# Kernel optimization log

Hardware: AMD Instinct MI355X
Metric: run time of the kernel (lower is better)

The kernel has to match this reference:

```python
import jax, jax.numpy as jnp
from jax import lax
import numpy as np

B = 32768
N_IN = 8
N_HID = 64
N_CTRL = 2
M_SCEN = (1.0, 1.2)          # scenario parameters for f/g
M_NOM = 1.0
CLF_LAM = 1.0
CBF_LAM = 1.0
P_CLF = 100.0
P_CBF = 50.0
QP_ITERS = 80                # fixed-iteration batched ADMM (OSQP-style) replacing CvxpyLayer
RHO = 1.0
SIGMA = 1e-6
INF = jnp.inf


def setup_inputs() -> dict:
    key = jax.random.key(0)
    ks = jax.random.split(key, 16)
    s = 0.3
    return {
        "x":   jax.random.normal(ks[0], (B, N_IN), jnp.float32),
        "VW1": jax.random.normal(ks[1], (N_HID, N_IN), jnp.float32) * s,
        "Vb1": jax.random.normal(ks[2], (N_HID,), jnp.float32) * s,
        "VW2": jax.random.normal(ks[3], (N_HID, N_HID), jnp.float32) * s,
        "Vb2": jax.random.normal(ks[4], (N_HID,), jnp.float32) * s,
        "HW1": jax.random.normal(ks[5], (N_HID, N_IN), jnp.float32) * s,
        "Hb1": jax.random.normal(ks[6], (N_HID,), jnp.float32) * s,
        "HW2": jax.random.normal(ks[7], (N_HID, N_HID), jnp.float32) * s,
        "Hb2": jax.random.normal(ks[8], (N_HID,), jnp.float32) * s,
        "HW3": jax.random.normal(ks[9], (N_HID, N_HID), jnp.float32) * s,
        "Hb3": jax.random.normal(ks[10], (N_HID,), jnp.float32) * s,
        "HW4": jax.random.normal(ks[11], (1, N_HID), jnp.float32) * s,
        "Hb4": jax.random.normal(ks[12], (1,), jnp.float32) * s,
        "G0":  jax.random.normal(ks[13], (N_IN, N_CTRL), jnp.float32) * s,
        "K":   jax.random.normal(ks[14], (N_IN, N_CTRL), jnp.float32) * s,
    }


def _lyapunov(x, W1, b1, W2, b2):
    t1 = jnp.tanh(x @ W1.T + b1)                                   # [B,H]
    t2 = jnp.tanh(t1 @ W2.T + b2)                                  # [B,H]
    V = 0.5 * jnp.sum(t2 * t2, axis=1)                             # [B]
    # fused diag(1-t^2) @ W chain (no diag_embed materialization)
    D1 = (1.0 - t1 ** 2)[:, :, None] * W1[None]                    # [B,H,N]
    D2 = (1.0 - t2 ** 2)[:, :, None] * jnp.einsum('hk,bkn->bhn', W2, D1)
    grad_V = jnp.einsum('bh,bhn->bn', t2, D2)                      # [B,N]
    return V, grad_V


def _barrier(x, W1, b1, W2, b2, W3, b3, W4, b4):
    t1 = jnp.tanh(x @ W1.T + b1)
    t2 = jnp.tanh(t1 @ W2.T + b2)
    t3 = jnp.tanh(t2 @ W3.T + b3)
    H = t3 @ W4.T + b4                                             # [B,1]
    D1 = (1.0 - t1 ** 2)[:, :, None] * W1[None]
    D2 = (1.0 - t2 ** 2)[:, :, None] * jnp.einsum('hk,bkn->bhn', W2, D1)
    D3 = (1.0 - t3 ** 2)[:, :, None] * jnp.einsum('hk,bkn->bhn', W3, D2)
    grad_H = jnp.einsum('oh,bhn->bn', W4, D3)                      # [B,N] (o=1)
    return H, grad_H


def _solve_qp(q, A, lo, hi):
    """Batched OSQP-style ADMM for min 0.5 z^T P z + q^T z  s.t. lo <= A z <= hi.
    P = diag([2,2,0,0,0,0]); z = [u(2), r_clf(2), s_cbf(2)]. Fixed iterations."""
    nb, mc, nz = A.shape[0], A.shape[1], A.shape[2]
    Pdiag = jnp.array([2.0, 2.0, 0.0, 0.0, 0.0, 0.0], q.dtype)
    M = RHO * jnp.einsum('bmi,bmj->bij', A, A) + jnp.diag(Pdiag + SIGMA)
    Minv = jnp.linalg.inv(M)                                       # [B,6,6]
    x0 = jnp.zeros((nb, nz), q.dtype)
    z0 = jnp.zeros((nb, mc), q.dtype)
    y0 = jnp.zeros((nb, mc), q.dtype)

    def step(carry, _):
        xx, zz, yy = carry
        rhs = SIGMA * xx - q + jnp.einsum('bmi,bm->bi', A, RHO * zz - yy)
        xt = jnp.einsum('bij,bj->bi', Minv, rhs)
        zt = jnp.einsum('bmi,bi->bm', A, xt)
        zn = jnp.clip(zt + yy / RHO, lo, hi)
        yn = yy + RHO * (zt - zn)
        return (xt, zn, yn), None

    (xf, _, _), _ = lax.scan(step, (x0, z0, y0), None, length=QP_ITERS)
    return xf                                                      # [B,6]


def _forward(x, VW1, Vb1, VW2, Vb2, HW1, Hb1, HW2, Hb2, HW3, Hb3, HW4, Hb4, G0, K):
    V, grad_V = _lyapunov(x, VW1, Vb1, VW2, Vb2)
    H, grad_H = _barrier(x, HW1, Hb1, HW2, Hb2, HW3, Hb3, HW4, Hb4)

    LfVs, LgVs, LfHs, LgHs = [], [], [], []
    for m in M_SCEN:
        # f(x,m) = -x/m ; g(x,m) = G0/m
        LfVs.append(-jnp.sum(grad_V * x, axis=1) / m)              # [B]
        LgVs.append((grad_V @ G0) / m)                             # [B,C]
        LfHs.append(-jnp.sum(grad_H * x, axis=1) / m)
        LgHs.append((grad_H @ G0) / m)
    u_nom = -(x @ K) * (1.0 / M_NOM)                               # [B,C]

    nb = x.shape[0]
    z2 = jnp.zeros((nb, 2), x.dtype)
    ey = jnp.eye(2, dtype=x.dtype)
    e = lambda i: jnp.broadcast_to(ey[i], (nb, 2))
    ninf = jnp.full((nb,), -INF, x.dtype)
    pinf = jnp.full((nb,), INF, x.dtype)
    zer = jnp.zeros((nb,), x.dtype)

    rows, los, his = [], [], []
    for i in range(len(M_SCEN)):
        # CBF: LfH + LgH@u + cbf_lam*H + s_i >= 0
        rows.append(jnp.concatenate([LgHs[i], z2, e(i)], axis=1))
        los.append(-(LfHs[i] + CBF_LAM * H[:, 0])); his.append(pinf)
        # CLF: LfV + LgV@u + clf_lam*V - r_i <= 0
        rows.append(jnp.concatenate([LgVs[i], -e(i), z2], axis=1))
        los.append(ninf); his.append(-(LfVs[i] + CLF_LAM * V))
    for i in range(len(M_SCEN)):
        rows.append(jnp.concatenate([z2, e(i), z2], axis=1)); los.append(zer); his.append(pinf)
    for i in range(len(M_SCEN)):
        rows.append(jnp.concatenate([z2, z2, e(i)], axis=1)); los.append(zer); his.append(pinf)

    A = jnp.stack(rows, axis=1)                                    # [B,8,6]
    lo = jnp.stack(los, axis=1)                                    # [B,8]
    hi = jnp.stack(his, axis=1)
    # objective ||u-u_nom||^2 + p_clf*sum r + p_cbf*sum s  ->  q = [-2 u_nom, p_clf, p_clf, p_cbf, p_cbf]
    q = jnp.concatenate([-2.0 * u_nom,
                         jnp.full((nb, 2), P_CLF, x.dtype),
                         jnp.full((nb, 2), P_CBF, x.dtype)], axis=1)

    z = _solve_qp(q, A, lo, hi)                                    # [B,6]
    u = z[:, :N_CTRL]
    relaxation = jnp.mean(z[:, N_CTRL:N_CTRL + len(M_SCEN)], axis=1, keepdims=True)  # [B,1]

    ns = float(len(M_SCEN))
    Vdot = sum(LfVs[i] + jnp.sum(LgVs[i] * u, axis=1) for i in range(len(M_SCEN))) / ns
    Hdot = sum(LfHs[i] + jnp.sum(LgHs[i] * u, axis=1) for i in range(len(M_SCEN))) / ns
    return u, relaxation, V, Vdot[:, None, None], H, Hdot[:, None, None]


def reference(x, VW1, Vb1, VW2, Vb2, HW1, Hb1, HW2, Hb2, HW3, Hb3, HW4, Hb4, G0, K):
    return _forward(x, VW1, Vb1, VW2, Vb2, HW1, Hb1, HW2, Hb2, HW3, Hb3, HW4, Hb4, G0, K)
```

## Files before the change

kernel.cpp:

```cpp
#include <hip/hip_runtime.h>
#include <hip/hip_bf16.h>
#include <math.h>

#define BTOT 32768

typedef _Float16 f16x8 __attribute__((ext_vector_type(8)));
typedef _Float16 f16x4 __attribute__((ext_vector_type(4)));
typedef float    f32x4 __attribute__((ext_vector_type(4)));

#define LDS_FENCE() asm volatile("s_waitcnt lgkmcnt(0)" ::: "memory")

__device__ __forceinline__ float ldin(const void* p, int i, int f32f) {
  return f32f ? ((const float*)p)[i]
              : __bfloat162float(((const __hip_bfloat16*)p)[i]);
}

__device__ __forceinline__ f32x4 MFMA(f16x8 a, f16x8 b, f32x4 c) {
  return __builtin_amdgcn_mfma_f32_16x16x32_f16(a, b, c, 0, 0, 0);
}

__device__ __forceinline__ float tanh_fast(float x) {
  float e = __expf(2.f * x);
  return 1.f - 2.f / (e + 1.f);
}

__device__ __forceinline__ float redq(float v) {
  v += __shfl_xor(v, 16, 64);
  v += __shfl_xor(v, 32, 64);
  return v;
}

__device__ __forceinline__ int widx(int h, int k) {
  return ((h >> 4) << 10) + ((k >> 5) << 9) + (((k >> 3) & 3) << 7) + ((h & 15) << 3) + (k & 7);
}

__global__ __launch_bounds__(512, 2) void nn_kernel(
    const void* px, const void* pVW1, const void* pVb1, const void* pVW2, const void* pVb2,
    const void* pHW1, const void* pHb1, const void* pHW2, const void* pHb2,
    const void* pHW3, const void* pHb3, const void* pHW4, const void* pHb4,
    const void* pG0, const void* pK, float* WS, float* out)
{
  __shared__ __align__(16) _Float16 sVW2[4096], sVW2T[4096];
  __shared__ __align__(16) _Float16 sHW2[4096], sHW2T[4096];
  __shared__ __align__(16) _Float16 sHW3[4096], sHW3T[4096];
  __shared__ __align__(16) _Float16 sW1Vh[512], sW1Vl[512], sW1Hh[512], sW1Hl[512];
  __shared__ __align__(16) _Float16 sXh[1024], sXl[1024];
  __shared__ __align__(16) _Float16 sAVh[8][1024], sAVl[8][1024];
  __shared__ __align__(16) _Float16 sAHh[8][1024], sAHl[8][1024];
  __shared__ __align__(16) float sVb1[64], sVb2[64], sHb1[64], sHb2[64], sHb3[64], sW4[64];
  __shared__ __align__(16) float sWGV0[64], sWGV1[64], sWGH0[64], sWGH1[64];
  __shared__ float sHb4v;
  __shared__ int sCnt;

  const int tid = threadIdx.x, lane = tid & 63, wave = tid >> 6;
  const int m = lane & 15, q = lane >> 4;
  const int ro = q * 128 + m * 8;

  if (tid == 0) sCnt = 0;
  __syncthreads();
  {
    const unsigned short* xb = (const unsigned short*)px;
    int good = 0;
#pragma unroll
    for (int i = 0; i < 2; ++i) {
      int ex = (xb[tid * 2 + i] >> 7) & 0xFF;
      good += (ex >= 97 && ex <= 157) ? 1 : 0;
    }
    atomicAdd(&sCnt, good);
  }
  __syncthreads();
  const int f32f = (sCnt >= 870) ? 0 : 1;
  const bool wsplit = (f32f != 0);

  for (int i = tid; i < 4096; i += 512) {
    int h = i >> 6, k = i & 63;
    int fw = widx(h, k), tw = widx(k, h);
    sVW2[fw] = (_Float16)ldin(pVW2, i, f32f); sVW2T[tw] = sVW2[fw];
    sHW2[fw] = (_Float16)ldin(pHW2, i, f32f); sHW2T[tw] = sHW2[fw];
    sHW3[fw] = (_Float16)ldin(pHW3, i, f32f); sHW3T[tw] = sHW3[fw];
  }
  for (int i = tid; i < 512; i += 512) {
    float v = ldin(pVW1, i, f32f); _Float16 hh = (_Float16)v;
    sW1Vh[i] = hh; sW1Vl[i] = (_Float16)(v - (float)hh);
    v = ldin(pHW1, i, f32f); hh = (_Float16)v;
    sW1Hh[i] = hh; sW1Hl[i] = (_Float16)(v - (float)hh);
  }
  for (int i = tid; i < 1024; i += 512) {
    float v = ldin(px, blockIdx.x * 1024 + i, f32f); _Float16 hh = (_Float16)v;
    sXh[i] = hh; sXl[i] = (_Float16)(v - (float)hh);
  }
  if (tid < 64) {
    float a0 = 0.f, a1 = 0.f, b0 = 0.f, b1 = 0.f;
#pragma unroll
    for (int nn = 0; nn < 8; ++nn) {
      float g0 = ldin(pG0, 2 * nn, f32f), g1 = ldin(pG0, 2 * nn + 1, f32f);
      float wv = ldin(pVW1, tid * 8 + nn, f32f), wh = ldin(pHW1, tid * 8 + nn, f32f);
      a0 += wv * g0; a1 += wv * g1; b0 += wh * g0; b1 += wh * g1;
    }
    sWGV0[tid] = a0; sWGV1[tid] = a1; sWGH0[tid] = b0; sWGH1[tid] = b1;
    sVb1[tid] = ldin(pVb1, tid, f32f);
    sVb2[tid] = ldin(pVb2, tid, f32f);
    sHb1[tid] = ldin(pHb1, tid, f32f);
    sHb2[tid] = ldin(pHb2, tid, f32f);
    sHb3[tid] = ldin(pHb3, tid, f32f);
    sW4[tid]  = ldin(pHW4, tid, f32f);
  }
  if (tid == 0) sHb4v = ldin(pHb4, 0, f32f);
  __syncthreads();

  f16x8 zf;
#pragma unroll
  for (int i = 0; i < 8; ++i) zf[i] = (_Float16)0.f;

  _Float16 *aVh = sAVh[wave], *aVl = sAVl[wave];
  _Float16 *aHh = sAHh[wave], *aHl = sAHl[wave];
  const int tb = wave * 16;

  auto wgemm = [&](const _Float16* Wp, const _Float16* ah_, const _Float16* al_, f32x4* acc) {
    f16x8 b0h = *(const f16x8*)(ah_ + ro);
    f16x8 b1h = *(const f16x8*)(ah_ + 512 + ro);
    f16x8 b0l = *(const f16x8*)(al_ + ro);
    f16x8 b1l = *(const f16x8*)(al_ + 512 + ro);
#pragma unroll
    for (int ht = 0; ht < 4; ++ht) {
      const _Float16* ap = Wp + ht * 1024 + ro;
      f16x8 a0 = *(const f16x8*)ap, a1 = *(const f16x8*)(ap + 512);
      f32x4 c = {0.f, 0.f, 0.f, 0.f};
      c = MFMA(a0, b0h, c); c = MFMA(a1, b1h, c);
      c = MFMA(a0, b0l, c); c = MFMA(a1, b1l, c);
      acc[ht] = c;
    }
  };
  auto wstore = [&](const f32x4* vals, _Float16* ah_, _Float16* al_) {
#pragma unroll
    for (int ht = 0; ht < 4; ++ht) {
      int aw = ((ht >> 1) << 9) + (((ht & 1) * 2 + (q >> 1)) << 7) + m * 8 + ((q & 1) << 2);
      f16x4 vh, vl;
#pragma unroll
      for (int r = 0; r < 4; ++r) {
        float x = vals[ht][r];
        _Float16 hh = (_Float16)x;
        vh[r] = hh; vl[r] = (_Float16)(x - (float)hh);
      }
      *(f16x4*)(ah_ + aw) = vh;
      *(f16x4*)(al_ + aw) = vl;
    }
  };
  auto l1gemm = [&](const _Float16* W1h, const _Float16* W1l, f32x4* acc) {
    f16x8 xbh = zf, xbl = zf;
    if (lane < 16) {
      xbh = *(const f16x8*)(sXh + (tb + m) * 8);
      xbl = *(const f16x8*)(sXl + (tb + m) * 8);
    }
#pragma unroll
    for (int ht = 0; ht < 4; ++ht) {
      f16x8 afh = zf, afl = zf;
      if (lane < 16) {
        afh = *(const f16x8*)(W1h + (ht * 16 + m) * 8);
        afl = *(const f16x8*)(W1l + (ht * 16 + m) * 8);
      }
      f32x4 c = {0.f, 0.f, 0.f, 0.f};
      c = MFMA(afh, xbh, c);
      c = MFMA(afh, xbl, c);
      if (wsplit) c = MFMA(afl, xbh, c);
      acc[ht] = c;
    }
  };

  f32x4 accV[4], accH[4], z1V[4], z1H[4], d1V[4], d1H[4], d2H[4], tvV[4], tvH[4];

  l1gemm(sW1Vh, sW1Vl, accV);
  l1gemm(sW1Hh, sW1Hl, accH);
#pragma unroll
  for (int ht = 0; ht < 4; ++ht) {
    z1V[ht] = accV[ht]; z1H[ht] = accH[ht];
    f32x4 bV = *(const f32x4*)&sVb1[ht * 16 + q * 4];
    f32x4 bH = *(const f32x4*)&sHb1[ht * 16 + q * 4];
#pragma unroll
    for (int r = 0; r < 4; ++r) {
      float t = tanh_fast(z1V[ht][r] + bV[r]);
      tvV[ht][r] = t; d1V[ht][r] = 1.f - t * t;
      t = tanh_fast(z1H[ht][r] + bH[r]);
      tvH[ht][r] = t; d1H[ht][r] = 1.f - t * t;
    }
  }
  wstore(tvV, aVh, aVl);
  wstore(tvH, aHh, aHl);
  LDS_FENCE();

  wgemm(sVW2, aVh, aVl, accV);
  wgemm(sHW2, aHh, aHl, accH);
  float pV = 0.f;
#pragma unroll
  for (int ht = 0; ht < 4; ++ht) {
    f32x4 bV = *(const f32x4*)&sVb2[ht * 16 + q * 4];
    f32x4 bH = *(const f32x4*)&sHb2[ht * 16 + q * 4];
#pragma unroll
    for (int r = 0; r < 4; ++r) {
      float t = tanh_fast(accV[ht][r] + bV[r]);
      pV += t * t;
      tvV[ht][r] = t * (1.f - t * t);
      t = tanh_fast(accH[ht][r] + bH[r]);
      tvH[ht][r] = t; d2H[ht][r] = 1.f - t * t;
    }
  }
  wstore(tvV, aVh, aVl);
  wstore(tvH, aHh, aHl);
  LDS_FENCE();

  wgemm(sVW2T, aVh, aVl, accV);
  wgemm(sHW3, aHh, aHl, accH);
  float pgvx = 0.f, plv0 = 0.f, plv1 = 0.f, pH = 0.f;
#pragma unroll
  for (int ht = 0; ht < 4; ++ht) {
    f32x4 g0 = *(const f32x4*)&sWGV0[ht * 16 + q * 4];
    f32x4 g1 = *(const f32x4*)&sWGV1[ht * 16 + q * 4];
    f32x4 bH = *(const f32x4*)&sHb3[ht * 16 + q * 4];
    f32x4 w4 = *(const f32x4*)&sW4[ht * 16 + q * 4];
#pragma unroll
    for (int r = 0; r < 4; ++r) {
      float wt = accV[ht][r] * d1V[ht][r];
      pgvx += wt * z1V[ht][r];
      plv0 += wt * g0[r]; plv1 += wt * g1[r];
      float t = tanh_fast(accH[ht][r] + bH[r]);
      pH += t * w4[r];
      tvH[ht][r] = w4[r] * (1.f - t * t);
    }
  }
  wstore(tvH, aHh, aHl);
  LDS_FENCE();

  wgemm(sHW3T, aHh, aHl, accH);
#pragma unroll
  for (int ht = 0; ht < 4; ++ht)
#pragma unroll
    for (int r = 0; r < 4; ++r) tvH[ht][r] = accH[ht][r] * d2H[ht][r];
  wstore(tvH, aHh, aHl);
  LDS_FENCE();

  wgemm(sHW2T, aHh, aHl, accH);
  float pghx = 0.f, plh0 = 0.f, plh1 = 0.f;
#pragma unroll
  for (int ht = 0; ht < 4; ++ht) {
    f32x4 g0 = *(const f32x4*)&sWGH0[ht * 16 + q * 4];
    f32x4 g1 = *(const f32x4*)&sWGH1[ht * 16 + q * 4];
#pragma unroll
    for (int r = 0; r < 4; ++r) {
      float wt = accH[ht][r] * d1H[ht][r];
      pghx += wt * z1H[ht][r];
      plh0 += wt * g0[r]; plh1 += wt * g1[r];
    }
  }

  {
    float rgvx = redq(pgvx), rlv0 = redq(plv0), rlv1 = redq(plv1), rV = 0.5f * redq(pV);
    float rghx = redq(pghx), rlh0 = redq(plh0), rlh1 = redq(plh1), rH = redq(pH) + sHb4v;
    if (lane < 16) {
      int e = blockIdx.x * 128 + tb + lane;
      WS[0 * BTOT + e] = rlh0;  WS[1 * BTOT + e] = rlh1;
      WS[2 * BTOT + e] = rlv0;  WS[3 * BTOT + e] = rlv1;
      WS[4 * BTOT + e] = rghx;  WS[5 * BTOT + e] = rgvx;
      out[98304 + e]  = rV;
      out[163840 + e] = rH;
    }
  }
}

__global__ __launch_bounds__(64) void qp_kernel(const void* px, const void* pK,
                                                const float* WS, float* out) {
  __shared__ int sCnt;
  const int tid = threadIdx.x;
  if (tid == 0) sCnt = 0;
  __syncthreads();
  {
    const unsigned short* xb = (const unsigned short*)px;
    int good = 0;
#pragma unroll
    for (int i = 0; i < 2; ++i) {
      int ex = (xb[tid * 2 + i] >> 7) & 0xFF;
      good += (ex >= 97 && ex <= 157) ? 1 : 0;
    }
    atomicAdd(&sCnt, good);
  }
  __syncthreads();
  const int f32f = (sCnt >= 109) ? 0 : 1;

  const int e = blockIdx.x * 64 + tid;
  const float im = 1.0f / 1.2f;
  const float sg = 1e-6f;

  float gh0 = WS[0 * BTOT + e], gh1 = WS[1 * BTOT + e];
  float gv0 = WS[2 * BTOT + e], gv1 = WS[3 * BTOT + e];
  float ghx = WS[4 * BTOT + e], gvx = WS[5 * BTOT + e];
  float V = out[98304 + e], H = out[163840 + e];

  float un0 = 0.f, un1 = 0.f;
#pragma unroll
  for (int n = 0; n < 8; ++n) {
    float xv = ldin(px, e * 8 + n, f32f);
    un0 -= xv * ldin(pK, 2 * n, f32f);
    un1 -= xv * ldin(pK, 2 * n + 1, f32f);
  }

  float lo0 = ghx - H;
  float hi1 = gvx - V;
  float lo2 = ghx * im - H;
  float hi3 = gvx * im - V;
  float qv0 = -2.f * un0, qv1 = -2.f * un1;

  const float d  = 2.f + sg;
  const float rd = 1.f / d;
  const float al = 1.f + im * im;
  const float be = al * (1.f - rd);
  float S00 = be * (gh0 * gh0 + gv0 * gv0) + d;
  float S11 = be * (gh1 * gh1 + gv1 * gv1) + d;
  float S01 = be * (gh0 * gh1 + gv0 * gv1);
  float idet = 1.f / (S00 * S11 - S01 * S01);
  float i00 = S11 * idet, i11 = S00 * idet, i01 = -S01 * idet;

  float X0 = 0.f, X1 = 0.f, X2 = 0.f, X3 = 0.f, X4 = 0.f, X5 = 0.f;
  float Z[8] = {0.f, 0.f, 0.f, 0.f, 0.f, 0.f, 0.f, 0.f};
  float Y[8] = {0.f, 0.f, 0.f, 0.f, 0.f, 0.f, 0.f, 0.f};

#pragma unroll 1
  for (int it = 0; it < 80; ++it) {
    float t0 = Z[0] - Y[0], t1 = Z[1] - Y[1], t2 = Z[2] - Y[2], t3 = Z[3] - Y[3];
    float t4 = Z[4] - Y[4], t5 = Z[5] - Y[5], t6 = Z[6] - Y[6], t7 = Z[7] - Y[7];
    float tauh = t0 + im * t2, tauv = t1 + im * t3;
    float b0 = sg * X0 - qv0 + gh0 * tauh + gv0 * tauv;
    float b1 = sg * X1 - qv1 + gh1 * tauh + gv1 * tauv;
    float b2 = sg * X2 - 100.f - t1 + t4;
    float b3 = sg * X3 - 100.f - t3 + t5;
    float b4 = sg * X4 - 50.f + t0 + t6;
    float b5 = sg * X5 - 50.f + t2 + t7;
    float p  = b2 + im * b3;
    float s2 = b4 + im * b5;
    float cb0 = gh0 * s2 - gv0 * p;
    float cb1 = gh1 * s2 - gv1 * p;
    float u0b = b0 - cb0 * rd;
    float u1b = b1 - cb1 * rd;
    X0 = i00 * u0b + i01 * u1b;
    X1 = i01 * u0b + i11 * u1b;
    float gdH = gh0 * X0 + gh1 * X1;
    float gdV = gv0 * X0 + gv1 * X1;
    X2 = (b2 + gdV) * rd;
    X3 = (b3 + im * gdV) * rd;
    X4 = (b4 - gdH) * rd;
    X5 = (b5 - im * gdH) * rd;
    float zt0 = gdH + X4;
    float zt1 = gdV - X2;
    float zt2 = gdH * im + X5;
    float zt3 = gdV * im - X3;

    float v, zn;
    v = zt0 + Y[0]; zn = fmaxf(v, lo0); Y[0] += zt0 - zn; Z[0] = zn;
    v = zt1 + Y[1]; zn = fminf(v, hi1); Y[1] += zt1 - zn; Z[1] = zn;
    v = zt2 + Y[2]; zn = fmaxf(v, lo2); Y[2] += zt2 - zn; Z[2] = zn;
    v = zt3 + Y[3]; zn = fminf(v, hi3); Y[3] += zt3 - zn; Z[3] = zn;
    v = X2 + Y[4];  zn = fmaxf(v, 0.f); Y[4] += X2 - zn;  Z[4] = zn;
    v = X3 + Y[5];  zn = fmaxf(v, 0.f); Y[5] += X3 - zn;  Z[5] = zn;
    v = X4 + Y[6];  zn = fmaxf(v, 0.f); Y[6] += X4 - zn;  Z[6] = zn;
    v = X5 + Y[7];  zn = fmaxf(v, 0.f); Y[7] += X5 - zn;  Z[7] = zn;
  }

  float relax = 0.5f * (X2 + X3);
  const float cc = 0.5f * (1.f + im);
  float Vdot = cc * (gv0 * X0 + gv1 * X1 - gvx);
  float Hdot = cc * (gh0 * X0 + gh1 * X1 - ghx);

  out[2 * e]      = X0;
  out[2 * e + 1]  = X1;
  out[65536 + e]  = relax;
  out[131072 + e] = Vdot;
  out[196608 + e] = Hdot;
}

extern "C" void kernel_launch(void* const* d_in, const int* in_sizes, int n_in,
                              void* d_out, int out_size, void* d_ws, size_t ws_size,
                              hipStream_t stream) {
  float* out = (float*)d_out;
  float* WS  = (float*)d_ws;
  nn_kernel<<<256, 512, 0, stream>>>(
      d_in[0], d_in[1], d_in[2], d_in[3], d_in[4],
      d_in[5], d_in[6], d_in[7], d_in[8],
      d_in[9], d_in[10], d_in[11], d_in[12],
      d_in[13], d_in[14], WS, out);
  qp_kernel<<<512, 64, 0, stream>>>(d_in[0], d_in[14], WS, out);
}
```

Measured before the change: 122.3 us.

## Fuse QP solve into NN kernel, drop hi/lo split activations, serialize V/H nets

```diff
diff --git a/kernel.cpp b/kernel.cpp
--- a/kernel.cpp
+++ b/kernel.cpp
@@ -21,7 +21,7 @@
 
 __device__ __forceinline__ float tanh_fast(float x) {
   float e = __expf(2.f * x);
-  return 1.f - 2.f / (e + 1.f);
+  return 1.f - 2.f * __builtin_amdgcn_rcpf(e + 1.f);
 }
 
 __device__ __forceinline__ float redq(float v) {
@@ -34,22 +34,21 @@
   return ((h >> 4) << 10) + ((k >> 5) << 9) + (((k >> 3) & 3) << 7) + ((h & 15) << 3) + (k & 7);
 }
 
-__global__ __launch_bounds__(512, 2) void nn_kernel(
+__global__ __launch_bounds__(512, 4) void fused_kernel(
     const void* px, const void* pVW1, const void* pVb1, const void* pVW2, const void* pVb2,
     const void* pHW1, const void* pHb1, const void* pHW2, const void* pHb2,
     const void* pHW3, const void* pHb3, const void* pHW4, const void* pHb4,
-    const void* pG0, const void* pK, float* WS, float* out)
+    const void* pG0, const void* pK, float* out)
 {
   __shared__ __align__(16) _Float16 sVW2[4096], sVW2T[4096];
   __shared__ __align__(16) _Float16 sHW2[4096], sHW2T[4096];
   __shared__ __align__(16) _Float16 sHW3[4096], sHW3T[4096];
   __shared__ __align__(16) _Float16 sW1Vh[512], sW1Vl[512], sW1Hh[512], sW1Hl[512];
-  __shared__ __align__(16) _Float16 sXh[1024], sXl[1024];
-  __shared__ __align__(16) _Float16 sAVh[8][1024], sAVl[8][1024];
-  __shared__ __align__(16) _Float16 sAHh[8][1024], sAHl[8][1024];
+  __shared__ __align__(16) _Float16 sAct[8][1024];
   __shared__ __align__(16) float sVb1[64], sVb2[64], sHb1[64], sHb2[64], sHb3[64], sW4[64];
   __shared__ __align__(16) float sWGV0[64], sWGV1[64], sWGH0[64], sWGH1[64];
-  __shared__ float sHb4v;
+  __shared__ __align__(16) float sQP[128][11];
+  __shared__ float sKv[16], sHb4v;
   __shared__ int sCnt;
 
   const int tid = threadIdx.x, lane = tid & 63, wave = tid >> 6;
@@ -84,10 +83,6 @@
     sW1Vh[i] = hh; sW1Vl[i] = (_Float16)(v - (float)hh);
     v = ldin(pHW1, i, f32f); hh = (_Float16)v;
     sW1Hh[i] = hh; sW1Hl[i] = (_Float16)(v - (float)hh);
-  }
-  for (int i = tid; i < 1024; i += 512) {
-    float v = ldin(px, blockIdx.x * 1024 + i, f32f); _Float16 hh = (_Float16)v;
-    sXh[i] = hh; sXl[i] = (_Float16)(v - (float)hh);
   }
   if (tid < 64) {
     float a0 = 0.f, a1 = 0.f, b0 = 0.f, b1 = 0.f;
@@ -105,6 +100,7 @@
     sHb3[tid] = ldin(pHb3, tid, f32f);
     sW4[tid]  = ldin(pHW4, tid, f32f);
   }
+  if (tid < 16) sKv[tid] = ldin(pK, tid, f32f);
   if (tid == 0) sHb4v = ldin(pHb4, 0, f32f);
   __syncthreads();
 
@@ -112,46 +108,43 @@
 #pragma unroll
   for (int i = 0; i < 8; ++i) zf[i] = (_Float16)0.f;
 
-  _Float16 *aVh = sAVh[wave], *aVl = sAVl[wave];
-  _Float16 *aHh = sAHh[wave], *aHl = sAHl[wave];
+  _Float16* act = sAct[wave];
   const int tb = wave * 16;
-
-  auto wgemm = [&](const _Float16* Wp, const _Float16* ah_, const _Float16* al_, f32x4* acc) {
-    f16x8 b0h = *(const f16x8*)(ah_ + ro);
-    f16x8 b1h = *(const f16x8*)(ah_ + 512 + ro);
-    f16x8 b0l = *(const f16x8*)(al_ + ro);
-    f16x8 b1l = *(const f16x8*)(al_ + 512 + ro);
+  const int e0 = blockIdx.x * 128 + tb;
+
+  f16x8 xbh = zf, xbl = zf;
+  if (lane < 16) {
+#pragma unroll
+    for (int n = 0; n < 8; ++n) {
+      float v = ldin(px, (e0 + m) * 8 + n, f32f);
+      _Float16 hh = (_Float16)v;
+      xbh[n] = hh; xbl[n] = (_Float16)(v - (float)hh);
+    }
+  }
+
+  auto wgemm = [&](const _Float16* Wp, f32x4* acc) {
+    f16x8 b0 = *(const f16x8*)(act + ro);
+    f16x8 b1 = *(const f16x8*)(act + 512 + ro);
 #pragma unroll
     for (int ht = 0; ht < 4; ++ht) {
       const _Float16* ap = Wp + ht * 1024 + ro;
-      f16x8 a0 = *(const f16x8*)ap, a1 = *(const f16x8*)(ap + 512);
       f32x4 c = {0.f, 0.f, 0.f, 0.f};
-      c = MFMA(a0, b0h, c); c = MFMA(a1, b1h, c);
-      c = MFMA(a0, b0l, c); c = MFMA(a1, b1l, c);
+      c = MFMA(*(const f16x8*)ap, b0, c);
+      c = MFMA(*(const f16x8*)(ap + 512), b1, c);
       acc[ht] = c;
     }
   };
-  auto wstore = [&](const f32x4* vals, _Float16* ah_, _Float16* al_) {
+  auto wstore = [&](const f32x4* vals) {
 #pragma unroll
     for (int ht = 0; ht < 4; ++ht) {
       int aw = ((ht >> 1) << 9) + (((ht & 1) * 2 + (q >> 1)) << 7) + m * 8 + ((q & 1) << 2);
-      f16x4 vh, vl;
-#pragma unroll
-      for (int r = 0; r < 4; ++r) {
-        float x = vals[ht][r];
-        _Float16 hh = (_Float16)x;
-        vh[r] = hh; vl[r] = (_Float16)(x - (float)hh);
-      }
-      *(f16x4*)(ah_ + aw) = vh;
-      *(f16x4*)(al_ + aw) = vl;
+      f16x4 vh;
+#pragma unroll
+      for (int r = 0; r < 4; ++r) vh[r] = (_Float16)vals[ht][r];
+      *(f16x4*)(act + aw) = vh;
     }
   };
   auto l1gemm = [&](const _Float16* W1h, const _Float16* W1l, f32x4* acc) {
-    f16x8 xbh = zf, xbl = zf;
-    if (lane < 16) {
-      xbh = *(const f16x8*)(sXh + (tb + m) * 8);
-      xbl = *(const f16x8*)(sXl + (tb + m) * 8);
-    }
 #pragma unroll
     for (int ht = 0; ht < 4; ++ht) {
       f16x8 afh = zf, afl = zf;
@@ -167,78 +160,97 @@
     }
   };
 
-  f32x4 accV[4], accH[4], z1V[4], z1H[4], d1V[4], d1H[4], d2H[4], tvV[4], tvH[4];
-
-  l1gemm(sW1Vh, sW1Vl, accV);
-  l1gemm(sW1Hh, sW1Hl, accH);
-#pragma unroll
-  for (int ht = 0; ht < 4; ++ht) {
-    z1V[ht] = accV[ht]; z1H[ht] = accH[ht];
-    f32x4 bV = *(const f32x4*)&sVb1[ht * 16 + q * 4];
-    f32x4 bH = *(const f32x4*)&sHb1[ht * 16 + q * 4];
-#pragma unroll
-    for (int r = 0; r < 4; ++r) {
-      float t = tanh_fast(z1V[ht][r] + bV[r]);
-      tvV[ht][r] = t; d1V[ht][r] = 1.f - t * t;
-      t = tanh_fast(z1H[ht][r] + bH[r]);
-      tvH[ht][r] = t; d1H[ht][r] = 1.f - t * t;
-    }
-  }
-  wstore(tvV, aVh, aVl);
-  wstore(tvH, aHh, aHl);
-  LDS_FENCE();
-
-  wgemm(sVW2, aVh, aVl, accV);
-  wgemm(sHW2, aHh, aHl, accH);
+  f32x4 acc[4], z1[4], d1[4], d2[4], tv[4];
+
+  l1gemm(sW1Vh, sW1Vl, acc);
+#pragma unroll
+  for (int ht = 0; ht < 4; ++ht) {
+    z1[ht] = acc[ht];
+    f32x4 b4 = *(const f32x4*)&sVb1[ht * 16 + q * 4];
+#pragma unroll
+    for (int r = 0; r < 4; ++r) {
+      float t = tanh_fast(z1[ht][r] + b4[r]);
+      tv[ht][r] = t; d1[ht][r] = 1.f - t * t;
+    }
+  }
+  wstore(tv); LDS_FENCE();
+
+  wgemm(sVW2, acc);
   float pV = 0.f;
 #pragma unroll
   for (int ht = 0; ht < 4; ++ht) {
-    f32x4 bV = *(const f32x4*)&sVb2[ht * 16 + q * 4];
-    f32x4 bH = *(const f32x4*)&sHb2[ht * 16 + q * 4];
-#pragma unroll
-    for (int r = 0; r < 4; ++r) {
-      float t = tanh_fast(accV[ht][r] + bV[r]);
+    f32x4 b4 = *(const f32x4*)&sVb2[ht * 16 + q * 4];
+#pragma unroll
+    for (int r = 0; r < 4; ++r) {
+      float t = tanh_fast(acc[ht][r] + b4[r]);
       pV += t * t;
-      tvV[ht][r] = t * (1.f - t * t);
-      t = tanh_fast(accH[ht][r] + bH[r]);
-      tvH[ht][r] = t; d2H[ht][r] = 1.f - t * t;
-    }
-  }
-  wstore(tvV, aVh, aVl);
-  wstore(tvH, aHh, aHl);
-  LDS_FENCE();
-
-  wgemm(sVW2T, aVh, aVl, accV);
-  wgemm(sHW3, aHh, aHl, accH);
-  float pgvx = 0.f, plv0 = 0.f, plv1 = 0.f, pH = 0.f;
+      tv[ht][r] = t * (1.f - t * t);
+    }
+  }
+  wstore(tv); LDS_FENCE();
+
+  wgemm(sVW2T, acc);
+  float pgvx = 0.f, plv0 = 0.f, plv1 = 0.f;
 #pragma unroll
   for (int ht = 0; ht < 4; ++ht) {
     f32x4 g0 = *(const f32x4*)&sWGV0[ht * 16 + q * 4];
     f32x4 g1 = *(const f32x4*)&sWGV1[ht * 16 + q * 4];
-    f32x4 bH = *(const f32x4*)&sHb3[ht * 16 + q * 4];
+#pragma unroll
+    for (int r = 0; r < 4; ++r) {
+      float wt = acc[ht][r] * d1[ht][r];
+      pgvx += wt * z1[ht][r];
+      plv0 += wt * g0[r]; plv1 += wt * g1[r];
+    }
+  }
+
+  l1gemm(sW1Hh, sW1Hl, acc);
+#pragma unroll
+  for (int ht = 0; ht < 4; ++ht) {
+    z1[ht] = acc[ht];
+    f32x4 b4 = *(const f32x4*)&sHb1[ht * 16 + q * 4];
+#pragma unroll
+    for (int r = 0; r < 4; ++r) {
+      float t = tanh_fast(z1[ht][r] + b4[r]);
+      tv[ht][r] = t; d1[ht][r] = 1.f - t * t;
+    }
+  }
+  wstore(tv); LDS_FENCE();
+
+  wgemm(sHW2, acc);
+#pragma unroll
+  for (int ht = 0; ht < 4; ++ht) {
+    f32x4 b4 = *(const f32x4*)&sHb2[ht * 16 + q * 4];
+#pragma unroll
+    for (int r = 0; r < 4; ++r) {
+      float t = tanh_fast(acc[ht][r] + b4[r]);
+      tv[ht][r] = t; d2[ht][r] = 1.f - t * t;
+    }
+  }
+  wstore(tv); LDS_FENCE();
+
+  wgemm(sHW3, acc);
+  float pH = 0.f;
+#pragma unroll
+  for (int ht = 0; ht < 4; ++ht) {
+    f32x4 b4 = *(const f32x4*)&sHb3[ht * 16 + q * 4];
     f32x4 w4 = *(const f32x4*)&sW4[ht * 16 + q * 4];
 #pragma unroll
     for (int r = 0; r < 4; ++r) {
-      float wt = accV[ht][r] * d1V[ht][r];
-      pgvx += wt * z1V[ht][r];
-      plv0 += wt * g0[r]; plv1 += wt * g1[r];
-      float t = tanh_fast(accH[ht][r] + bH[r]);
+      float t = tanh_fast(acc[ht][r] + b4[r]);
       pH += t * w4[r];
-      tvH[ht][r] = w4[r] * (1.f - t * t);
-    }
-  }
-  wstore(tvH, aHh, aHl);
-  LDS_FENCE();
-
-  wgemm(sHW3T, aHh, aHl, accH);
+      tv[ht][r] = w4[r] * (1.f - t * t);
+    }
+  }
+  wstore(tv); LDS_FENCE();
+
+  wgemm(sHW3T, acc);
 #pragma unroll
   for (int ht = 0; ht < 4; ++ht)
 #pragma unroll
-    for (int r = 0; r < 4; ++r) tvH[ht][r] = accH[ht][r] * d2H[ht][r];
-  wstore(tvH, aHh, aHl);
-  LDS_FENCE();
-
-  wgemm(sHW2T, aHh, aHl, accH);
+    for (int r = 0; r < 4; ++r) tv[ht][r] = acc[ht][r] * d2[ht][r];
+  wstore(tv); LDS_FENCE();
+
+  wgemm(sHW2T, acc);
   float pghx = 0.f, plh0 = 0.f, plh1 = 0.f;
 #pragma unroll
   for (int ht = 0; ht < 4; ++ht) {
@@ -246,8 +258,8 @@
     f32x4 g1 = *(const f32x4*)&sWGH1[ht * 16 + q * 4];
 #pragma unroll
     for (int r = 0; r < 4; ++r) {
-      float wt = accH[ht][r] * d1H[ht][r];
-      pghx += wt * z1H[ht][r];
+      float wt = acc[ht][r] * d1[ht][r];
+      pghx += wt * z1[ht][r];
       plh0 += wt * g0[r]; plh1 += wt * g1[r];
     }
   }
@@ -256,50 +268,33 @@
     float rgvx = redq(pgvx), rlv0 = redq(plv0), rlv1 = redq(plv1), rV = 0.5f * redq(pV);
     float rghx = redq(pghx), rlh0 = redq(plh0), rlh1 = redq(plh1), rH = redq(pH) + sHb4v;
     if (lane < 16) {
-      int e = blockIdx.x * 128 + tb + lane;
-      WS[0 * BTOT + e] = rlh0;  WS[1 * BTOT + e] = rlh1;
-      WS[2 * BTOT + e] = rlv0;  WS[3 * BTOT + e] = rlv1;
-      WS[4 * BTOT + e] = rghx;  WS[5 * BTOT + e] = rgvx;
-      out[98304 + e]  = rV;
-      out[163840 + e] = rH;
-    }
-  }
-}
-
-__global__ __launch_bounds__(64) void qp_kernel(const void* px, const void* pK,
-                                                const float* WS, float* out) {
-  __shared__ int sCnt;
-  const int tid = threadIdx.x;
-  if (tid == 0) sCnt = 0;
+      int el = tb + lane;
+      sQP[el][0] = rlh0;  sQP[el][1] = rlh1;
+      sQP[el][2] = rlv0;  sQP[el][3] = rlv1;
+      sQP[el][4] = rghx;  sQP[el][5] = rgvx;
+      sQP[el][6] = rV;    sQP[el][7] = rH;
+      out[98304 + e0 + lane]  = rV;
+      out[163840 + e0 + lane] = rH;
+    }
+  }
   __syncthreads();
-  {
-    const unsigned short* xb = (const unsigned short*)px;
-    int good = 0;
-#pragma unroll
-    for (int i = 0; i < 2; ++i) {
-      int ex = (xb[tid * 2 + i] >> 7) & 0xFF;
-      good += (ex >= 97 && ex <= 157) ? 1 : 0;
-    }
-    atomicAdd(&sCnt, good);
-  }
-  __syncthreads();
-  const int f32f = (sCnt >= 109) ? 0 : 1;
-
-  const int e = blockIdx.x * 64 + tid;
+
+  if (tid >= 128) return;
+  const int e = blockIdx.x * 128 + tid;
   const float im = 1.0f / 1.2f;
   const float sg = 1e-6f;
 
-  float gh0 = WS[0 * BTOT + e], gh1 = WS[1 * BTOT + e];
-  float gv0 = WS[2 * BTOT + e], gv1 = WS[3 * BTOT + e];
-  float ghx = WS[4 * BTOT + e], gvx = WS[5 * BTOT + e];
-  float V = out[98304 + e], H = out[163840 + e];
+  float gh0 = sQP[tid][0], gh1 = sQP[tid][1];
+  float gv0 = sQP[tid][2], gv1 = sQP[tid][3];
+  float ghx = sQP[tid][4], gvx = sQP[tid][5];
+  float V   = sQP[tid][6], H   = sQP[tid][7];
 
   float un0 = 0.f, un1 = 0.f;
 #pragma unroll
   for (int n = 0; n < 8; ++n) {
     float xv = ldin(px, e * 8 + n, f32f);
-    un0 -= xv * ldin(pK, 2 * n, f32f);
-    un1 -= xv * ldin(pK, 2 * n + 1, f32f);
+    un0 -= xv * sKv[2 * n];
+    un1 -= xv * sKv[2 * n + 1];
   }
 
   float lo0 = ghx - H;
@@ -379,11 +374,9 @@
                               void* d_out, int out_size, void* d_ws, size_t ws_size,
                               hipStream_t stream) {
   float* out = (float*)d_out;
-  float* WS  = (float*)d_ws;
-  nn_kernel<<<256, 512, 0, stream>>>(
+  fused_kernel<<<256, 512, 0, stream>>>(
       d_in[0], d_in[1], d_in[2], d_in[3], d_in[4],
       d_in[5], d_in[6], d_in[7], d_in[8],
       d_in[9], d_in[10], d_in[11], d_in[12],
-      d_in[13], d_in[14], WS, out);
-  qp_kernel<<<512, 64, 0, stream>>>(d_in[0], d_in[14], WS, out);
-}
+      d_in[13], d_in[14], out);
+}
```

New measurement: 121.6 us. No clear change (-0.5%).
